# Optimization experiments

Hardware: AMD Instinct MI355X
Metric: run time of the kernel (lower is better)

## Reference

```python
import jax, jax.numpy as jnp
import numpy as np

EPSILON = 1e-15
N_IN = 1_000_000          # number of input variables
M = 2_000_000             # nodes per internal layer
FANIN = 4
E = M * FANIN             # edges per layer
S0 = 2 * N_IN + 2         # encoded input size
LOG2 = float(np.log(2.0))


def _make_structure():
    rng = np.random.default_rng(0)
    in_sizes = [S0, M, M, M]
    ptrs = [jnp.asarray(rng.integers(0, s, size=E), dtype=jnp.int32) for s in in_sizes]
    csr = jnp.asarray(np.repeat(np.arange(M, dtype=np.int32), FANIN))  # unrolled CSR, fan-in 4
    return ptrs, csr


def log1mexp(x):
    # log(1 - exp(x)) for x <= 0, numerically stable (Maechler 2012)
    mask = x > -LOG2
    x_hi = jnp.where(mask, x, -1.0)   # branch-safe inputs
    x_lo = jnp.where(mask, -1.0, x)
    return jnp.where(mask, jnp.log(-jnp.expm1(x_hi)), jnp.log1p(-jnp.exp(x_lo)))


def encode_input(pos):
    neg = log1mexp(pos)
    interleaved = jnp.stack([pos, neg], axis=1).reshape(-1)  # [2N] = pos/neg interleaved
    head = jnp.array([-jnp.inf, 0.0], dtype=pos.dtype)       # literals False, True
    return jnp.concatenate([head, interleaved])              # [2N+2]


def product_layer(x, ptrs, csr):
    # sum of log-probs per segment (product in prob space)
    return jax.ops.segment_sum(x[ptrs], csr, num_segments=M)


def sum_layer(x, ptrs, csr):
    # segmented logsumexp with EPSILON floor, max detached (torch no_grad)
    g = x[ptrs]
    m = jax.lax.stop_gradient(jax.ops.segment_max(g, csr, num_segments=M))
    e = jnp.nan_to_num(jnp.exp(g - m[csr]), nan=0.0, posinf=jnp.inf, neginf=-jnp.inf)
    s = jax.ops.segment_sum(e, csr, num_segments=M) + EPSILON
    return jnp.log(s) + m


def setup_inputs() -> dict:
    key = jax.random.key(0)
    u = jax.random.uniform(key, (N_IN,), dtype=jnp.float32, minval=1e-6, maxval=1.0)
    pos = jnp.log(u)  # log-probabilities, strictly < 0
    (p0, p1, p2, p3), csr = _make_structure()
    return {"pos": pos, "ptrs0": p0, "ptrs1": p1, "ptrs2": p2, "ptrs3": p3, "csr": csr}


def reference(pos, ptrs0, ptrs1, ptrs2, ptrs3, csr):
    x = encode_input(pos)
    x = product_layer(x, ptrs0, csr)
    x = sum_layer(x, ptrs1, csr)
    x = product_layer(x, ptrs2, csr)
    x = sum_layer(x, ptrs3, csr)
    return x
```

## Files before the change

### kernel.cpp

```cpp
#include <hip/hip_runtime.h>
#include <hip/hip_fp16.h>
#include <math.h>


#define LOG2F 0.6931471805599453f

typedef int iv4 __attribute__((ext_vector_type(4)));

__global__ void encode_kernel(const float* __restrict__ pos,
                              __half* __restrict__ x0, int n) {
    int i = blockIdx.x * blockDim.x + threadIdx.x;
    if (i == 0) { x0[0] = __float2half(-INFINITY); x0[1] = __float2half(0.0f); }
    if (i < n) {
        float p = pos[i];
        float neg = (p > -LOG2F) ? logf(-expm1f(p)) : log1pf(-expf(p));
        __half2 v;
        v.x = __float2half(p);
        v.y = __float2half(neg);
        ((__half2*)(x0 + 2))[i] = v;
    }
}

__global__ void product_kernel(const __half* __restrict__ x,
                               const iv4* __restrict__ ptrs,
                               __half* __restrict__ out, int m) {
    int i = blockIdx.x * blockDim.x + threadIdx.x;
    if (i < m) {
        iv4 p = __builtin_nontemporal_load(&ptrs[i]);
        float s = __half2float(x[p.x]) + __half2float(x[p.y])
                + __half2float(x[p.z]) + __half2float(x[p.w]);
        __builtin_nontemporal_store(__half_as_short(__float2half(s)),
                                    (short*)&out[i]);
    }
}

template <typename OutT>
__global__ void sum_kernel(const __half* __restrict__ x,
                           const iv4* __restrict__ ptrs,
                           OutT* __restrict__ out, int m) {
    int i = blockIdx.x * blockDim.x + threadIdx.x;
    if (i < m) {
        iv4 p = __builtin_nontemporal_load(&ptrs[i]);
        float a = __half2float(x[p.x]), b = __half2float(x[p.y]);
        float c = __half2float(x[p.z]), d = __half2float(x[p.w]);
        float mx = fmaxf(fmaxf(a, b), fmaxf(c, d));
        float ea = expf(a - mx); ea = (ea != ea) ? 0.0f : ea;
        float eb = expf(b - mx); eb = (eb != eb) ? 0.0f : eb;
        float ec = expf(c - mx); ec = (ec != ec) ? 0.0f : ec;
        float ed = expf(d - mx); ed = (ed != ed) ? 0.0f : ed;
        float s = ea + eb + ec + ed + 1e-15f;
        float r = logf(s) + mx;
        if constexpr (sizeof(OutT) == 2) {
            __builtin_nontemporal_store(__half_as_short(__float2half(r)),
                                        (short*)&out[i]);
        } else {
            __builtin_nontemporal_store(r, (float*)&out[i]);
        }
    }
}

extern "C" void kernel_launch(void* const* d_in, const int* in_sizes, int n_in,
                              void* d_out, int out_size, void* d_ws, size_t ws_size,
                              hipStream_t stream) {
    const float* pos = (const float*)d_in[0];
    const iv4*   p0  = (const iv4*)d_in[1];
    const iv4*   p1  = (const iv4*)d_in[2];
    const iv4*   p2  = (const iv4*)d_in[3];
    const iv4*   p3  = (const iv4*)d_in[4];

    const int N = in_sizes[0];
    const int M = out_size;

    char* ws = (char*)d_ws;
    size_t s0_bytes = (((size_t)(2 * (size_t)N + 2) * sizeof(__half)) + 255) & ~(size_t)255;
    size_t m_bytes  = (((size_t)M * sizeof(__half)) + 255) & ~(size_t)255;
    __half* x0 = (__half*)ws;
    __half* x1 = (__half*)(ws + s0_bytes);
    __half* x2 = (__half*)(ws + s0_bytes + m_bytes);
    float* outp = (float*)d_out;

    const int blk = 256;
    const int gN = (N + blk - 1) / blk;
    const int gM = (M + blk - 1) / blk;

    encode_kernel          <<<gN, blk, 0, stream>>>(pos, x0, N);
    product_kernel         <<<gM, blk, 0, stream>>>(x0, p0, x1, M);
    sum_kernel<__half>     <<<gM, blk, 0, stream>>>(x1, p1, x2, M);
    product_kernel         <<<gM, blk, 0, stream>>>(x2, p2, x1, M);
    sum_kernel<float>      <<<gM, blk, 0, stream>>>(x1, p3, outp, M);
}
```

Before: 307.8 us.

## Fuse all layers into one persistent cooperative kernel with grid syncs

Replaces the five separate launches with a single cooperative persistent kernel that runs encode and the four layers in sequence, separated by grid-wide barriers. Each thread processes four nodes per iteration so more gathers are in flight, and the sum layer switches to fast __expf/__logf intrinsics. This removes per-launch overhead and inter-kernel drain gaps, at the cost of grid.sync barriers and a grid limited to occupancy, which may reduce memory-level parallelism compared with oversubscribed launches.

```diff
diff --git a/kernel.cpp b/kernel.cpp
--- a/kernel.cpp
+++ b/kernel.cpp
@@ -1,62 +1,93 @@
 #include <hip/hip_runtime.h>
 #include <hip/hip_fp16.h>
+#include <hip/hip_cooperative_groups.h>
 #include <math.h>
 
 
 #define LOG2F 0.6931471805599453f
 
+namespace cg = cooperative_groups;
+
 typedef int iv4 __attribute__((ext_vector_type(4)));
 
-__global__ void encode_kernel(const float* __restrict__ pos,
-                              __half* __restrict__ x0, int n) {
-    int i = blockIdx.x * blockDim.x + threadIdx.x;
-    if (i == 0) { x0[0] = __float2half(-INFINITY); x0[1] = __float2half(0.0f); }
-    if (i < n) {
-        float p = pos[i];
-        float neg = (p > -LOG2F) ? logf(-expm1f(p)) : log1pf(-expf(p));
-        __half2 v;
-        v.x = __float2half(p);
-        v.y = __float2half(neg);
-        ((__half2*)(x0 + 2))[i] = v;
+template <bool IS_SUM, typename OutT>
+__device__ __forceinline__ void run_layer(const __half* __restrict__ x,
+                                          const iv4* __restrict__ ptrs,
+                                          OutT* __restrict__ out,
+                                          int m, int tid, int T) {
+    for (int base = tid; base < m; base += 4 * T) {
+        iv4 p[4];
+#pragma unroll
+        for (int u = 0; u < 4; ++u) {
+            int i = base + u * T;
+            p[u] = __builtin_nontemporal_load(&ptrs[(i < m) ? i : base]);
+        }
+        float g[4][4];
+#pragma unroll
+        for (int u = 0; u < 4; ++u) {
+            g[u][0] = __half2float(x[p[u].x]);
+            g[u][1] = __half2float(x[p[u].y]);
+            g[u][2] = __half2float(x[p[u].z]);
+            g[u][3] = __half2float(x[p[u].w]);
+        }
+#pragma unroll
+        for (int u = 0; u < 4; ++u) {
+            int i = base + u * T;
+            if (i < m) {
+                float r;
+                if constexpr (IS_SUM) {
+                    float mx = fmaxf(fmaxf(g[u][0], g[u][1]), fmaxf(g[u][2], g[u][3]));
+                    float e0 = __expf(g[u][0] - mx); e0 = (e0 != e0) ? 0.0f : e0;
+                    float e1 = __expf(g[u][1] - mx); e1 = (e1 != e1) ? 0.0f : e1;
+                    float e2 = __expf(g[u][2] - mx); e2 = (e2 != e2) ? 0.0f : e2;
+                    float e3 = __expf(g[u][3] - mx); e3 = (e3 != e3) ? 0.0f : e3;
+                    r = __logf(e0 + e1 + e2 + e3 + 1e-15f) + mx;
+                } else {
+                    r = g[u][0] + g[u][1] + g[u][2] + g[u][3];
+                }
+                if constexpr (sizeof(OutT) == 2) {
+                    __builtin_nontemporal_store(__half_as_short(__float2half(r)),
+                                                (short*)&out[i]);
+                } else {
+                    __builtin_nontemporal_store(r, (float*)&out[i]);
+                }
+            }
+        }
     }
 }
 
-__global__ void product_kernel(const __half* __restrict__ x,
-                               const iv4* __restrict__ ptrs,
-                               __half* __restrict__ out, int m) {
-    int i = blockIdx.x * blockDim.x + threadIdx.x;
-    if (i < m) {
-        iv4 p = __builtin_nontemporal_load(&ptrs[i]);
-        float s = __half2float(x[p.x]) + __half2float(x[p.y])
-                + __half2float(x[p.z]) + __half2float(x[p.w]);
-        __builtin_nontemporal_store(__half_as_short(__float2half(s)),
-                                    (short*)&out[i]);
+__global__ void __launch_bounds__(256)
+fused_kernel(const float* __restrict__ pos,
+             const iv4* __restrict__ p0, const iv4* __restrict__ p1,
+             const iv4* __restrict__ p2, const iv4* __restrict__ p3,
+             __half* __restrict__ x0, __half* __restrict__ x1,
+             __half* __restrict__ x2, float* __restrict__ outp,
+             int n, int m) {
+    cg::grid_group grid = cg::this_grid();
+    const int T = (int)(gridDim.x * blockDim.x);
+    const int tid = (int)(blockIdx.x * blockDim.x + threadIdx.x);
+
+    if (tid == 0) {
+        x0[0] = __float2half(-INFINITY);
+        x0[1] = __float2half(0.0f);
     }
-}
+    for (int i = tid; i < n; i += T) {
+        float pv = __builtin_nontemporal_load(&pos[i]);
+        float neg = (pv > -LOG2F) ? logf(-expm1f(pv)) : log1pf(-expf(pv));
+        unsigned int packed =
+            ((unsigned int)__half_as_ushort(__float2half(neg)) << 16) |
+            (unsigned int)__half_as_ushort(__float2half(pv));
+        __builtin_nontemporal_store(packed, (unsigned int*)(x0 + 2) + i);
+    }
+    grid.sync();
 
-template <typename OutT>
-__global__ void sum_kernel(const __half* __restrict__ x,
-                           const iv4* __restrict__ ptrs,
-                           OutT* __restrict__ out, int m) {
-    int i = blockIdx.x * blockDim.x + threadIdx.x;
-    if (i < m) {
-        iv4 p = __builtin_nontemporal_load(&ptrs[i]);
-        float a = __half2float(x[p.x]), b = __half2float(x[p.y]);
-        float c = __half2float(x[p.z]), d = __half2float(x[p.w]);
-        float mx = fmaxf(fmaxf(a, b), fmaxf(c, d));
-        float ea = expf(a - mx); ea = (ea != ea) ? 0.0f : ea;
-        float eb = expf(b - mx); eb = (eb != eb) ? 0.0f : eb;
-        float ec = expf(c - mx); ec = (ec != ec) ? 0.0f : ec;
-        float ed = expf(d - mx); ed = (ed != ed) ? 0.0f : ed;
-        float s = ea + eb + ec + ed + 1e-15f;
-        float r = logf(s) + mx;
-        if constexpr (sizeof(OutT) == 2) {
-            __builtin_nontemporal_store(__half_as_short(__float2half(r)),
-                                        (short*)&out[i]);
-        } else {
-            __builtin_nontemporal_store(r, (float*)&out[i]);
-        }
-    }
+    run_layer<false, __half>(x0, p0, x1, m, tid, T);
+    grid.sync();
+    run_layer<true, __half>(x1, p1, x2, m, tid, T);
+    grid.sync();
+    run_layer<false, __half>(x2, p2, x1, m, tid, T);
+    grid.sync();
+    run_layer<true, float>(x1, p3, outp, m, tid, T);
 }
 
 extern "C" void kernel_launch(void* const* d_in, const int* in_sizes, int n_in,
@@ -68,8 +99,8 @@
     const iv4*   p2  = (const iv4*)d_in[3];
     const iv4*   p3  = (const iv4*)d_in[4];
 
-    const int N = in_sizes[0];
-    const int M = out_size;
+    int N = in_sizes[0];
+    int M = out_size;
 
     char* ws = (char*)d_ws;
     size_t s0_bytes = (((size_t)(2 * (size_t)N + 2) * sizeof(__half)) + 255) & ~(size_t)255;
@@ -79,13 +110,26 @@
     __half* x2 = (__half*)(ws + s0_bytes + m_bytes);
     float* outp = (float*)d_out;
 
-    const int blk = 256;
-    const int gN = (N + blk - 1) / blk;
-    const int gM = (M + blk - 1) / blk;
+    static int nblk = 0;
+    if (nblk == 0) {
+        int bpc = 0;
+        hipError_t e = hipOccupancyMaxActiveBlocksPerMultiprocessor(
+            &bpc, reinterpret_cast<const void*>(fused_kernel), 256, 0);
+        int ncu = 256;
+        int dev = 0;
+        if (hipGetDevice(&dev) == hipSuccess) {
+            hipDeviceProp_t prop{};
+            if (hipGetDeviceProperties(&prop, dev) == hipSuccess &&
+                prop.multiProcessorCount > 0) {
+                ncu = prop.multiProcessorCount;
+            }
+        }
+        nblk = (e == hipSuccess && bpc >= 1) ? bpc * ncu : 2048;
+    }
 
-    encode_kernel          <<<gN, blk, 0, stream>>>(pos, x0, N);
-    product_kernel         <<<gM, blk, 0, stream>>>(x0, p0, x1, M);
-    sum_kernel<__half>     <<<gM, blk, 0, stream>>>(x1, p1, x2, M);
-    product_kernel         <<<gM, blk, 0, stream>>>(x2, p2, x1, M);
-    sum_kernel<float>      <<<gM, blk, 0, stream>>>(x1, p3, outp, M);
+    void* args[] = {(void*)&pos, (void*)&p0, (void*)&p1, (void*)&p2, (void*)&p3,
+                    (void*)&x0, (void*)&x1, (void*)&x2, (void*)&outp,
+                    (void*)&N, (void*)&M};
+    hipLaunchCooperativeKernel(reinterpret_cast<const void*>(fused_kernel),
+                               dim3(nblk), dim3(256), args, 0, stream);
 }
```

New measurement: 1.174 ms. 3.81x slower.
